# Optimization experiments

Measured on AMD Instinct MI355X. Metric: run time of the kernel, lower is better.

The kernel has to match this reference:

```python
import jax, jax.numpy as jnp
import numpy as np

N_NODES = 50000
FEAT_DIM = 256
HIDDEN = 64
CLASS_DIM = 64
N_EDGES = 800000
K_HOPS = 2


def setup_inputs() -> dict:
    key = jax.random.key(0)
    k1, k2, k3, k4, k5, k6 = jax.random.split(key, 6)
    x = jax.random.normal(k1, (N_NODES, FEAT_DIM), dtype=jnp.float32)
    edge_rows = jax.random.randint(k2, (N_EDGES,), 0, N_NODES, dtype=jnp.int32)
    edge_cols = jax.random.randint(k3, (N_EDGES,), 0, N_NODES, dtype=jnp.int32)
    edge_vals = jax.random.uniform(k4, (N_EDGES,), dtype=jnp.float32)  # normalized-adj values (>0)
    # xavier_uniform-style init scale
    lim_e = float(np.sqrt(6.0 / (FEAT_DIM + HIDDEN)))
    lim_c = float(np.sqrt(6.0 / (7 * HIDDEN + CLASS_DIM)))
    w_embed = jax.random.uniform(k5, (FEAT_DIM, HIDDEN), dtype=jnp.float32, minval=-lim_e, maxval=lim_e)
    w_classify = jax.random.uniform(k6, (7 * HIDDEN, CLASS_DIM), dtype=jnp.float32, minval=-lim_c, maxval=lim_c)
    return {"x": x, "edge_rows": edge_rows, "edge_cols": edge_cols,
            "edge_vals": edge_vals, "w_embed": w_embed, "w_classify": w_classify}


def reference(x, edge_rows, edge_cols, edge_vals, w_embed, w_classify):
    # Node_GCN forward (eval mode; dropout inert).
    # a1 = adj - I, a2 = adj@adj - adj - I  =>
    #   a1 @ r = s - r,   a2 @ r = adj@s - s - r   with s = adj @ r
    n = x.shape[0]

    def spmm(r):  # adj @ r via edge-list gather + segment-sum: [n, d]
        return jax.ops.segment_sum(edge_vals[:, None] * r[edge_cols], edge_rows, num_segments=n)

    act = jax.nn.relu
    r = act(x @ w_embed)                  # [n, h]
    rs = [r]
    for _ in range(K_HOPS):
        s = spmm(r)                       # adj @ r
        t = spmm(s)                       # adj @ adj @ r
        r1 = s - r                        # a1 @ r
        r2 = t - s - r                    # a2 @ r
        r = act(jnp.concatenate([r1, r2], axis=1))  # width doubles each hop
        rs.append(r)
    r_final = jnp.concatenate(rs, axis=1)  # [n, 7h]
    return jax.nn.softmax(r_final @ w_classify, axis=1)
```

## Files before the change

### kernel.cpp

```cpp
#include <hip/hip_runtime.h>

#define N_NODES 50000
#define NPAD 50048
#define FEAT 256
#define HID 64
#define NEDGE 800000
#define SCAN_CHUNK 2048
#define NB_SCAN 25
#define NB_EDGE 3125
#define NB_GEMM 391

typedef unsigned short bf16_t;
typedef __attribute__((ext_vector_type(8))) short bf16x8;
typedef __attribute__((ext_vector_type(4))) float f32x4;

#define MFMA_BF16 __builtin_amdgcn_mfma_f32_16x16x32_bf16

__device__ __forceinline__ bf16_t f2bf(float f) {
    union { float f; unsigned u; } v; v.f = f;
    unsigned r = v.u + 0x7fff + ((v.u >> 16) & 1);
    return (bf16_t)(r >> 16);
}
__device__ __forceinline__ void unpack2(unsigned u, float& lo, float& hi) {
    union { unsigned u; float f; } a, b;
    a.u = u << 16; b.u = u & 0xffff0000u;
    lo = a.f; hi = b.f;
}
__device__ __forceinline__ unsigned pack2(float lo, float hi) {
    return ((unsigned)f2bf(lo)) | (((unsigned)f2bf(hi)) << 16);
}

__device__ __forceinline__ void pack_w_body(const float* __restrict__ wsrc,
        bf16_t* __restrict__ wdst, int idx) {
    int lane = idx & 63, nt = (idx >> 6) & 3, ks = idx >> 8;
    int kb  = ks * 32 + ((lane >> 4) * 8);
    int col = nt * 16 + (lane & 15);
    unsigned p[4];
#pragma unroll
    for (int j = 0; j < 4; ++j)
        p[j] = pack2(wsrc[(size_t)(kb + 2*j) * 64 + col],
                     wsrc[(size_t)(kb + 2*j + 1) * 64 + col]);
    uint4 u; u.x = p[0]; u.y = p[1]; u.z = p[2]; u.w = p[3];
    *(uint4*)(wdst + (size_t)idx * 8) = u;
}

__global__ __launch_bounds__(256) void prep_kernel(const int* __restrict__ rows,
        int* __restrict__ cnt, const float* __restrict__ we, bf16_t* __restrict__ wep,
        const float* __restrict__ wc, bf16_t* __restrict__ wcp) {
    const int b = blockIdx.x, t = threadIdx.x;
    if (b < NB_EDGE) {
        int e = b * 256 + t;
        if (e < NEDGE) atomicAdd(&cnt[rows[e]], 1);
    } else if (b < NB_EDGE + 8) {
        pack_w_body(we, wep, (b - NB_EDGE) * 256 + t);
    } else {
        pack_w_body(wc, wcp, (b - NB_EDGE - 8) * 256 + t);
    }
}

__global__ __launch_bounds__(256) void scan_a(const int* __restrict__ cnt,
        int* __restrict__ bsum) {
    __shared__ int sd[256];
    const int t = threadIdx.x;
    const int base = blockIdx.x * SCAN_CHUNK + t * 8;
    int s = 0;
#pragma unroll
    for (int i = 0; i < 8; ++i) {
        int idx = base + i;
        s += (idx < N_NODES) ? cnt[idx] : 0;
    }
    sd[t] = s; __syncthreads();
    for (int off = 128; off > 0; off >>= 1) {
        if (t < off) sd[t] += sd[t + off];
        __syncthreads();
    }
    if (t == 0) bsum[blockIdx.x] = sd[0];
}

__global__ __launch_bounds__(256) void scan_c(const int* __restrict__ cnt,
        const int* __restrict__ bsum, int* __restrict__ rowPtr,
        int* __restrict__ fill) {
    __shared__ int sd[256];
    __shared__ int sboff;
    const int t = threadIdx.x;
    const int base = blockIdx.x * SCAN_CHUNK + t * 8;
    if (t == 0) {
        int a = 0, tot = 0;
        for (int b = 0; b < NB_SCAN; ++b) {
            int v = bsum[b];
            if (b < (int)blockIdx.x) a += v;
            tot += v;
        }
        sboff = a;
        if (blockIdx.x == NB_SCAN - 1) rowPtr[N_NODES] = tot;
    }
    int v[8];
    int s = 0;
#pragma unroll
    for (int i = 0; i < 8; ++i) {
        int idx = base + i;
        v[i] = (idx < N_NODES) ? cnt[idx] : 0;
        s += v[i];
    }
    sd[t] = s; __syncthreads();
    for (int off = 1; off < 256; off <<= 1) {
        int add = (t >= off) ? sd[t - off] : 0;
        __syncthreads();
        sd[t] += add;
        __syncthreads();
    }
    int run = sboff + (sd[t] - s);
#pragma unroll
    for (int i = 0; i < 8; ++i) {
        int idx = base + i;
        if (idx < N_NODES) { rowPtr[idx] = run; fill[idx] = 0; }
        run += v[i];
    }
}

__global__ __launch_bounds__(256) void scatter_embed_kernel(
        const int* __restrict__ rows, const int* __restrict__ cols,
        const float* __restrict__ vals, const int* __restrict__ rowPtr,
        int* __restrict__ fill, uint2* __restrict__ colval,
        const float* __restrict__ x, const bf16_t* __restrict__ wep,
        bf16_t* __restrict__ r0) {
    if (blockIdx.x < NB_EDGE) {
        int e = blockIdx.x * 256 + threadIdx.x;
        if (e < NEDGE) {
            int r = rows[e];
            int p = rowPtr[r] + atomicAdd(&fill[r], 1);
            uint2 cv; cv.x = (unsigned)cols[e]; cv.y = __float_as_uint(vals[e]);
            colval[p] = cv;
        }
        return;
    }
    const int blk = blockIdx.x - NB_EDGE;
    const int t = threadIdx.x;
    const int l = t & 63, w = t >> 6;
    const int lm = l & 15, lg = l >> 4;
    const int base = blk * 128 + w * 32;

    int m0 = base + lm, m1 = base + 16 + lm;
    if (m0 >= N_NODES) m0 = N_NODES - 1;
    if (m1 >= N_NODES) m1 = N_NODES - 1;
    const float* xp0 = x + (size_t)m0 * FEAT + lg * 8;
    const float* xp1 = x + (size_t)m1 * FEAT + lg * 8;

    f32x4 acc[2][4];
#pragma unroll
    for (int i = 0; i < 2; ++i)
#pragma unroll
        for (int j = 0; j < 4; ++j) acc[i][j] = (f32x4){0.f, 0.f, 0.f, 0.f};

    auto aload = [&](const float* p) {
        float4 u0 = *(const float4*)(p);
        float4 u1 = *(const float4*)(p + 4);
        bf16x8 r;
        r[0] = (short)f2bf(u0.x); r[1] = (short)f2bf(u0.y);
        r[2] = (short)f2bf(u0.z); r[3] = (short)f2bf(u0.w);
        r[4] = (short)f2bf(u1.x); r[5] = (short)f2bf(u1.y);
        r[6] = (short)f2bf(u1.z); r[7] = (short)f2bf(u1.w);
        return r;
    };
    auto wb = [&](int ks, int nt) {
        return *(const bf16x8*)(wep + ((size_t)(ks * 4 + nt) * 64 + l) * 8);
    };

    const int NK = FEAT / 32;
    bf16x8 a0 = aload(xp0), a1 = aload(xp1);
    bf16x8 b0 = wb(0,0), b1 = wb(0,1), b2 = wb(0,2), b3 = wb(0,3);
    for (int ks = 0; ks < NK; ++ks) {
        bf16x8 na0, na1, nb0, nb1, nb2, nb3;
        const bool more = (ks + 1 < NK);
        if (more) {
            int kt = (ks + 1) * 32;
            na0 = aload(xp0 + kt); na1 = aload(xp1 + kt);
            nb0 = wb(ks+1,0); nb1 = wb(ks+1,1); nb2 = wb(ks+1,2); nb3 = wb(ks+1,3);
        }
        acc[0][0] = MFMA_BF16(a0, b0, acc[0][0], 0, 0, 0);
        acc[1][0] = MFMA_BF16(a1, b0, acc[1][0], 0, 0, 0);
        acc[0][1] = MFMA_BF16(a0, b1, acc[0][1], 0, 0, 0);
        acc[1][1] = MFMA_BF16(a1, b1, acc[1][1], 0, 0, 0);
        acc[0][2] = MFMA_BF16(a0, b2, acc[0][2], 0, 0, 0);
        acc[1][2] = MFMA_BF16(a1, b2, acc[1][2], 0, 0, 0);
        acc[0][3] = MFMA_BF16(a0, b3, acc[0][3], 0, 0, 0);
        acc[1][3] = MFMA_BF16(a1, b3, acc[1][3], 0, 0, 0);
        if (more) { a0 = na0; a1 = na1; b0 = nb0; b1 = nb1; b2 = nb2; b3 = nb3; }
    }

#pragma unroll
    for (int rt = 0; rt < 2; ++rt)
#pragma unroll
        for (int r = 0; r < 4; ++r) {
            int R = base + rt * 16 + lg * 4 + r;
            if (R < N_NODES) {
                bf16_t* o = r0 + (size_t)R * HID + lm;
                o[0]  = f2bf(fmaxf(acc[rt][0][r], 0.f));
                o[16] = f2bf(fmaxf(acc[rt][1][r], 0.f));
                o[32] = f2bf(fmaxf(acc[rt][2][r], 0.f));
                o[48] = f2bf(fmaxf(acc[rt][3][r], 0.f));
            }
        }
}

__global__ __launch_bounds__(256) void spmm64_kernel(const uint2* __restrict__ colval,
        const int* __restrict__ rowPtr,
        const bf16_t* __restrict__ src, bf16_t* __restrict__ dst) {
    const int l = threadIdx.x & 63;
    const int c = l & 31, h = l >> 5;
    const int row  = (int)((blockIdx.x * 256u + threadIdx.x) >> 6);
    const int beg = rowPtr[row], end = rowPtr[row + 1];
    const unsigned* srcu = (const unsigned*)src;
    float a0 = 0.f, a1 = 0.f;
    int i = beg;
    for (; i + 16 <= end; i += 16) {
        uint2 cv[8]; unsigned g[8];
#pragma unroll
        for (int j = 0; j < 8; ++j) cv[j] = colval[i + 2*j + h];
#pragma unroll
        for (int j = 0; j < 8; ++j) g[j] = srcu[(size_t)cv[j].x * 32 + c];
#pragma unroll
        for (int j = 0; j < 8; ++j) {
            float lo, hi; unpack2(g[j], lo, hi);
            float v = __uint_as_float(cv[j].y);
            a0 += v*lo; a1 += v*hi;
        }
    }
    for (; i + 2 <= end; i += 2) {
        uint2 cv = colval[i + h];
        float lo, hi; unpack2(srcu[(size_t)cv.x*32 + c], lo, hi);
        float v = __uint_as_float(cv.y);
        a0 += v*lo; a1 += v*hi;
    }
    if (i + h < end) {
        uint2 cv = colval[i + h];
        float lo, hi; unpack2(srcu[(size_t)cv.x*32 + c], lo, hi);
        float v = __uint_as_float(cv.y);
        a0 += v*lo; a1 += v*hi;
    }
    a0 += __shfl_xor(a0, 32);
    a1 += __shfl_xor(a1, 32);
    if (h == 0)
        ((unsigned*)dst)[(size_t)row*32 + c] = pack2(a0, a1);
}

__global__ __launch_bounds__(256) void spmm64f_kernel(const uint2* __restrict__ colval,
        const int* __restrict__ rowPtr,
        const bf16_t* __restrict__ s, const bf16_t* __restrict__ r0,
        bf16_t* __restrict__ r1c) {
    const int l = threadIdx.x & 63;
    const int c = l & 31, h = l >> 5;
    const int row  = (int)((blockIdx.x * 256u + threadIdx.x) >> 6);
    const int beg = rowPtr[row], end = rowPtr[row + 1];
    const unsigned* su = (const unsigned*)s;
    const unsigned* r0u = (const unsigned*)r0;
    float a0 = 0.f, a1 = 0.f;
    int i = beg;
    for (; i + 16 <= end; i += 16) {
        uint2 cv[8]; unsigned g[8];
#pragma unroll
        for (int j = 0; j < 8; ++j) cv[j] = colval[i + 2*j + h];
#pragma unroll
        for (int j = 0; j < 8; ++j) g[j] = su[(size_t)cv[j].x * 32 + c];
#pragma unroll
        for (int j = 0; j < 8; ++j) {
            float lo, hi; unpack2(g[j], lo, hi);
            float v = __uint_as_float(cv[j].y);
            a0 += v*lo; a1 += v*hi;
        }
    }
    for (; i + 2 <= end; i += 2) {
        uint2 cv = colval[i + h];
        float lo, hi; unpack2(su[(size_t)cv.x*32 + c], lo, hi);
        float v = __uint_as_float(cv.y);
        a0 += v*lo; a1 += v*hi;
    }
    if (i + h < end) {
        uint2 cv = colval[i + h];
        float lo, hi; unpack2(su[(size_t)cv.x*32 + c], lo, hi);
        float v = __uint_as_float(cv.y);
        a0 += v*lo; a1 += v*hi;
    }
    a0 += __shfl_xor(a0, 32);
    a1 += __shfl_xor(a1, 32);
    if (h == 0) {
        float sv0, sv1, rv0, rv1;
        unpack2(su[(size_t)row*32 + c], sv0, sv1);
        unpack2(r0u[(size_t)row*32 + c], rv0, rv1);
        unsigned* r1u = (unsigned*)r1c;
        r1u[(size_t)row*64 + c]      = pack2(fmaxf(sv0 - rv0, 0.f), fmaxf(sv1 - rv1, 0.f));
        r1u[(size_t)row*64 + 32 + c] = pack2(fmaxf(a0 - sv0 - rv0, 0.f), fmaxf(a1 - sv1 - rv1, 0.f));
    }
}

__global__ __launch_bounds__(256) void spmm128_kernel(const uint2* __restrict__ colval,
        const int* __restrict__ rowPtr,
        const bf16_t* __restrict__ src, bf16_t* __restrict__ dst) {
    const int lane = threadIdx.x & 63;
    const int row  = (int)((blockIdx.x * 256u + threadIdx.x) >> 6);
    const int beg = rowPtr[row], end = rowPtr[row + 1];
    const unsigned* srcu = (const unsigned*)src;
    float a0 = 0.f, a1 = 0.f;
    int i = beg;
    for (; i + 8 <= end; i += 8) {
        uint2 cv[8]; unsigned u[8];
#pragma unroll
        for (int j = 0; j < 8; ++j) cv[j] = colval[i+j];
#pragma unroll
        for (int j = 0; j < 8; ++j) u[j] = srcu[(size_t)cv[j].x*64 + lane];
#pragma unroll
        for (int j = 0; j < 8; ++j) {
            float lo, hi; unpack2(u[j], lo, hi);
            float v = __uint_as_float(cv[j].y);
            a0 += v*lo; a1 += v*hi;
        }
    }
    for (; i < end; ++i) {
        uint2 cv = colval[i];
        float lo, hi; unpack2(srcu[(size_t)cv.x*64 + lane], lo, hi);
        float v = __uint_as_float(cv.y);
        a0 += v*lo; a1 += v*hi;
    }
    ((unsigned*)dst)[(size_t)row*64 + lane] = pack2(a0, a1);
}

__global__ __launch_bounds__(256) void spmm128f_kernel(const uint2* __restrict__ colval,
        const int* __restrict__ rowPtr,
        const bf16_t* __restrict__ s2, const bf16_t* __restrict__ r1,
        bf16_t* __restrict__ r2c) {
    const int lane = threadIdx.x & 63;
    const int row  = (int)((blockIdx.x * 256u + threadIdx.x) >> 6);
    const int beg = rowPtr[row], end = rowPtr[row + 1];
    const unsigned* s2u = (const unsigned*)s2;
    const unsigned* r1u = (const unsigned*)r1;
    float a0 = 0.f, a1 = 0.f;
    int i = beg;
    for (; i + 8 <= end; i += 8) {
        uint2 cv[8]; unsigned u[8];
#pragma unroll
        for (int j = 0; j < 8; ++j) cv[j] = colval[i+j];
#pragma unroll
        for (int j = 0; j < 8; ++j) u[j] = s2u[(size_t)cv[j].x*64 + lane];
#pragma unroll
        for (int j = 0; j < 8; ++j) {
            float lo, hi; unpack2(u[j], lo, hi);
            float v = __uint_as_float(cv[j].y);
            a0 += v*lo; a1 += v*hi;
        }
    }
    for (; i < end; ++i) {
        uint2 cv = colval[i];
        float lo, hi; unpack2(s2u[(size_t)cv.x*64 + lane], lo, hi);
        float v = __uint_as_float(cv.y);
        a0 += v*lo; a1 += v*hi;
    }
    float s0v, s1v, r0v, r1v;
    unpack2(s2u[(size_t)row*64 + lane], s0v, s1v);
    unpack2(r1u[(size_t)row*64 + lane], r0v, r1v);
    unsigned* r2u = (unsigned*)r2c;
    r2u[(size_t)row*128 + lane]      = pack2(fmaxf(s0v - r0v, 0.f), fmaxf(s1v - r1v, 0.f));
    r2u[(size_t)row*128 + 64 + lane] = pack2(fmaxf(a0 - s0v - r0v, 0.f), fmaxf(a1 - s1v - r1v, 0.f));
}

__global__ __launch_bounds__(256) void classify_mfma(const bf16_t* __restrict__ r0,
        const bf16_t* __restrict__ r1, const bf16_t* __restrict__ r2,
        const bf16_t* __restrict__ wcp, float* __restrict__ out) {
    const int t = threadIdx.x;
    const int l = t & 63, w = t >> 6;
    const int lm = l & 15, lg = l >> 4;
    const int base = blockIdx.x * 128 + w * 32;

    const int m0 = base + lm, m1 = base + 16 + lm;
    const bf16_t* p0_r0 = r0 + (size_t)m0 * 64  + lg * 8;
    const bf16_t* p0_r1 = r1 + (size_t)m0 * 128 + lg * 8;
    const bf16_t* p0_r2 = r2 + (size_t)m0 * 256 + lg * 8;
    const bf16_t* p1_r0 = r0 + (size_t)m1 * 64  + lg * 8;
    const bf16_t* p1_r1 = r1 + (size_t)m1 * 128 + lg * 8;
    const bf16_t* p1_r2 = r2 + (size_t)m1 * 256 + lg * 8;

    f32x4 acc[2][4];
#pragma unroll
    for (int i = 0; i < 2; ++i)
#pragma unroll
        for (int j = 0; j < 4; ++j) acc[i][j] = (f32x4){0.f, 0.f, 0.f, 0.f};

    auto aload = [&](const bf16_t* pr0, const bf16_t* pr1, const bf16_t* pr2, int kt) {
        const bf16_t* p = (kt < 64) ? (pr0 + kt) : (kt < 192) ? (pr1 + kt - 64) : (pr2 + kt - 192);
        return *(const bf16x8*)p;
    };
    auto wb = [&](int ks, int nt) {
        return *(const bf16x8*)(wcp + ((size_t)(ks * 4 + nt) * 64 + l) * 8);
    };

    const int NK = 14;
    bf16x8 a0 = aload(p0_r0, p0_r1, p0_r2, 0);
    bf16x8 a1 = aload(p1_r0, p1_r1, p1_r2, 0);
    bf16x8 b0 = wb(0,0), b1 = wb(0,1), b2 = wb(0,2), b3 = wb(0,3);
    for (int ks = 0; ks < NK; ++ks) {
        bf16x8 na0, na1, nb0, nb1, nb2, nb3;
        const bool more = (ks + 1 < NK);
        if (more) {
            int kt = (ks + 1) * 32;
            na0 = aload(p0_r0, p0_r1, p0_r2, kt);
            na1 = aload(p1_r0, p1_r1, p1_r2, kt);
            nb0 = wb(ks+1,0); nb1 = wb(ks+1,1); nb2 = wb(ks+1,2); nb3 = wb(ks+1,3);
        }
        acc[0][0] = MFMA_BF16(a0, b0, acc[0][0], 0, 0, 0);
        acc[1][0] = MFMA_BF16(a1, b0, acc[1][0], 0, 0, 0);
        acc[0][1] = MFMA_BF16(a0, b1, acc[0][1], 0, 0, 0);
        acc[1][1] = MFMA_BF16(a1, b1, acc[1][1], 0, 0, 0);
        acc[0][2] = MFMA_BF16(a0, b2, acc[0][2], 0, 0, 0);
        acc[1][2] = MFMA_BF16(a1, b2, acc[1][2], 0, 0, 0);
        acc[0][3] = MFMA_BF16(a0, b3, acc[0][3], 0, 0, 0);
        acc[1][3] = MFMA_BF16(a1, b3, acc[1][3], 0, 0, 0);
        if (more) { a0 = na0; a1 = na1; b0 = nb0; b1 = nb1; b2 = nb2; b3 = nb3; }
    }

#pragma unroll
    for (int rt = 0; rt < 2; ++rt)
#pragma unroll
        for (int r = 0; r < 4; ++r) {
            float v0 = acc[rt][0][r], v1 = acc[rt][1][r];
            float v2 = acc[rt][2][r], v3 = acc[rt][3][r];
            float m = fmaxf(fmaxf(v0, v1), fmaxf(v2, v3));
#pragma unroll
            for (int o = 1; o < 16; o <<= 1) m = fmaxf(m, __shfl_xor(m, o));
            float e0 = __expf(v0 - m), e1 = __expf(v1 - m);
            float e2 = __expf(v2 - m), e3 = __expf(v3 - m);
            float s = e0 + e1 + e2 + e3;
#pragma unroll
            for (int o = 1; o < 16; o <<= 1) s += __shfl_xor(s, o);
            float inv = 1.f / s;
            int R = base + rt * 16 + lg * 4 + r;
            if (R < N_NODES) {
                float* o = out + (size_t)R * 64 + lm;
                o[0]  = e0 * inv;
                o[16] = e1 * inv;
                o[32] = e2 * inv;
                o[48] = e3 * inv;
            }
        }
}

extern "C" void kernel_launch(void* const* d_in, const int* in_sizes, int n_in,
                              void* d_out, int out_size, void* d_ws, size_t ws_size,
                              hipStream_t stream) {
    const float* x    = (const float*)d_in[0];
    const int*   erow = (const int*)d_in[1];
    const int*   ecol = (const int*)d_in[2];
    const float* eval = (const float*)d_in[3];
    const float* we   = (const float*)d_in[4];
    const float* wc   = (const float*)d_in[5];
    float* out = (float*)d_out;

    char* wsp = (char*)d_ws;
    size_t off = 0;
    auto take = [&](size_t bytes) {
        char* p = wsp + off;
        off += (bytes + 255) & ~(size_t)255;
        return p;
    };
    bf16_t* r0     = (bf16_t*)take((size_t)NPAD * 64 * 2);
    bf16_t* sbuf   = (bf16_t*)take((size_t)NPAD * 128 * 2);
    bf16_t* r1c    = (bf16_t*)take((size_t)NPAD * 128 * 2);
    bf16_t* r2c    = (bf16_t*)take((size_t)NPAD * 256 * 2);
    int*    cnt    = (int*)take((size_t)N_NODES * 4);
    int*    rowPtr = (int*)take((size_t)(N_NODES + 1) * 4);
    int*    fill   = (int*)take((size_t)N_NODES * 4);
    int*    bsum   = (int*)take((size_t)NB_SCAN * 4);
    uint2*  colval = (uint2*)take((size_t)NEDGE * 8);
    bf16_t* wep    = (bf16_t*)take((size_t)8  * 256 * 8 * 2);
    bf16_t* wcp    = (bf16_t*)take((size_t)14 * 256 * 8 * 2);
    (void)ws_size; (void)in_sizes; (void)n_in; (void)out_size;

    hipMemsetAsync(cnt, 0, (size_t)N_NODES * 4, stream);

    prep_kernel<<<NB_EDGE + 8 + 14, 256, 0, stream>>>(erow, cnt, we, wep, wc, wcp);
    scan_a<<<NB_SCAN, 256, 0, stream>>>(cnt, bsum);
    scan_c<<<NB_SCAN, 256, 0, stream>>>(cnt, bsum, rowPtr, fill);
    scatter_embed_kernel<<<NB_EDGE + NB_GEMM, 256, 0, stream>>>(
        erow, ecol, eval, rowPtr, fill, colval, x, wep, r0);

    spmm64_kernel <<<12500, 256, 0, stream>>>(colval, rowPtr, r0, sbuf);
    spmm64f_kernel<<<12500, 256, 0, stream>>>(colval, rowPtr, sbuf, r0, r1c);
    spmm128_kernel<<<12500, 256, 0, stream>>>(colval, rowPtr, r1c, sbuf);
    spmm128f_kernel<<<12500, 256, 0, stream>>>(colval, rowPtr, sbuf, r1c, r2c);

    classify_mfma<<<NB_GEMM, 256, 0, stream>>>(r0, r1c, r2c, wcp, out);
}
```

Measured before the change: 271.5 us.

## Build CSR via two-level bucketing to reduce global atomic scatter cost

Edges are first scattered into coarse buckets of four rows using a per-bucket atomic counter and staged in temporary arrays. A new kernel then sorts each 128-row range into its final CSR position with shared-memory atomics. The aim is to spread out contention on per-row global atomics and make the final colval writes more local. The cost is an extra kernel launch and an extra pass that reads and writes all the edges.

```diff
diff --git a/kernel.cpp b/kernel.cpp
--- a/kernel.cpp
+++ b/kernel.cpp
@@ -9,6 +9,9 @@
 #define NB_SCAN 25
 #define NB_EDGE 3125
 #define NB_GEMM 391
+#define NBKT_FINE 12500
+#define RPB 128
+#define NBKT_CSR 391
 
 typedef unsigned short bf16_t;
 typedef __attribute__((ext_vector_type(8))) short bf16x8;
@@ -79,7 +82,7 @@
 
 __global__ __launch_bounds__(256) void scan_c(const int* __restrict__ cnt,
         const int* __restrict__ bsum, int* __restrict__ rowPtr,
-        int* __restrict__ fill) {
+        int* __restrict__ bfill) {
     __shared__ int sd[256];
     __shared__ int sboff;
     const int t = threadIdx.x;
@@ -113,24 +116,29 @@
 #pragma unroll
     for (int i = 0; i < 8; ++i) {
         int idx = base + i;
-        if (idx < N_NODES) { rowPtr[idx] = run; fill[idx] = 0; }
+        if (idx < N_NODES) {
+            rowPtr[idx] = run;
+            if (idx < NBKT_FINE) bfill[idx] = 0;
+        }
         run += v[i];
     }
 }
 
-__global__ __launch_bounds__(256) void scatter_embed_kernel(
+__global__ __launch_bounds__(256) void bin_embed_kernel(
         const int* __restrict__ rows, const int* __restrict__ cols,
         const float* __restrict__ vals, const int* __restrict__ rowPtr,
-        int* __restrict__ fill, uint2* __restrict__ colval,
+        int* __restrict__ bfill, int* __restrict__ tmpR, uint2* __restrict__ tmpCV,
         const float* __restrict__ x, const bf16_t* __restrict__ wep,
         bf16_t* __restrict__ r0) {
     if (blockIdx.x < NB_EDGE) {
         int e = blockIdx.x * 256 + threadIdx.x;
         if (e < NEDGE) {
             int r = rows[e];
-            int p = rowPtr[r] + atomicAdd(&fill[r], 1);
+            int b = r >> 2;
+            int p = rowPtr[b << 2] + atomicAdd(&bfill[b], 1);
+            tmpR[p] = r;
             uint2 cv; cv.x = (unsigned)cols[e]; cv.y = __float_as_uint(vals[e]);
-            colval[p] = cv;
+            tmpCV[p] = cv;
         }
         return;
     }
@@ -201,6 +209,41 @@
                 o[48] = f2bf(fmaxf(acc[rt][3][r], 0.f));
             }
         }
+}
+
+__global__ __launch_bounds__(256) void bucket_csr_kernel(const int* __restrict__ rowPtr,
+        const int* __restrict__ tmpR, const uint2* __restrict__ tmpCV,
+        uint2* __restrict__ colval) {
+    __shared__ int cnt[RPB];
+    __shared__ int off[RPB];
+    const int t = threadIdx.x;
+    const int b = blockIdx.x;
+    const int r0 = b << 7;
+    const int r1 = (r0 + RPB < N_NODES) ? (r0 + RPB) : N_NODES;
+    const int base = rowPtr[r0];
+    const int nE = rowPtr[r1] - base;
+
+    if (t < RPB) cnt[t] = 0;
+    __syncthreads();
+    for (int i = t; i < nE; i += 256)
+        atomicAdd(&cnt[tmpR[base + i] - r0], 1);
+    __syncthreads();
+    if (t < RPB) off[t] = cnt[t];
+    __syncthreads();
+    for (int d = 1; d < RPB; d <<= 1) {
+        int v = 0;
+        if (t < RPB && t >= d) v = off[t - d];
+        __syncthreads();
+        if (t < RPB) off[t] += v;
+        __syncthreads();
+    }
+    if (t < RPB) off[t] -= cnt[t];
+    __syncthreads();
+    for (int i = t; i < nE; i += 256) {
+        int r = tmpR[base + i];
+        int p = atomicAdd(&off[r - r0], 1);
+        colval[base + p] = tmpCV[base + i];
+    }
 }
 
 __global__ __launch_bounds__(256) void spmm64_kernel(const uint2* __restrict__ colval,
@@ -466,9 +509,11 @@
     bf16_t* r2c    = (bf16_t*)take((size_t)NPAD * 256 * 2);
     int*    cnt    = (int*)take((size_t)N_NODES * 4);
     int*    rowPtr = (int*)take((size_t)(N_NODES + 1) * 4);
-    int*    fill   = (int*)take((size_t)N_NODES * 4);
+    int*    bfill  = (int*)take((size_t)NBKT_FINE * 4);
     int*    bsum   = (int*)take((size_t)NB_SCAN * 4);
     uint2*  colval = (uint2*)take((size_t)NEDGE * 8);
+    int*    tmpR   = (int*)take((size_t)NEDGE * 4);
+    uint2*  tmpCV  = (uint2*)take((size_t)NEDGE * 8);
     bf16_t* wep    = (bf16_t*)take((size_t)8  * 256 * 8 * 2);
     bf16_t* wcp    = (bf16_t*)take((size_t)14 * 256 * 8 * 2);
     (void)ws_size; (void)in_sizes; (void)n_in; (void)out_size;
@@ -477,9 +522,10 @@
 
     prep_kernel<<<NB_EDGE + 8 + 14, 256, 0, stream>>>(erow, cnt, we, wep, wc, wcp);
     scan_a<<<NB_SCAN, 256, 0, stream>>>(cnt, bsum);
-    scan_c<<<NB_SCAN, 256, 0, stream>>>(cnt, bsum, rowPtr, fill);
-    scatter_embed_kernel<<<NB_EDGE + NB_GEMM, 256, 0, stream>>>(
-        erow, ecol, eval, rowPtr, fill, colval, x, wep, r0);
+    scan_c<<<NB_SCAN, 256, 0, stream>>>(cnt, bsum, rowPtr, bfill);
+    bin_embed_kernel<<<NB_EDGE + NB_GEMM, 256, 0, stream>>>(
+        erow, ecol, eval, rowPtr, bfill, tmpR, tmpCV, x, wep, r0);
+    bucket_csr_kernel<<<NBKT_CSR, 256, 0, stream>>>(rowPtr, tmpR, tmpCV, colval);
 
     spmm64_kernel <<<12500, 256, 0, stream>>>(colval, rowPtr, r0, sbuf);
     spmm64f_kernel<<<12500, 256, 0, stream>>>(colval, rowPtr, sbuf, r0, r1c);
```

Measured after the change: 303.1 us. 1.12x slower.
